# Kernel optimization log

Measured on AMD Instinct MI355X. Metric: run time of the kernel, lower is better.

## Reference

```python
import jax, jax.numpy as jnp
import numpy as np

GS = 256          # group_size
KER = 17          # depthwise conv kernel size (MossFormer ConvModule)

def layer_norm(x, g, b):
    mu = jnp.mean(x, -1, keepdims=True)
    var = jnp.mean(jnp.square(x - mu), -1, keepdims=True)
    return (x - mu) * jax.lax.rsqrt(var + 1e-5) * g + b

def dwconv(x, kernel):
    # x: (B, N, C), kernel: (C, 1, K); depthwise 'same' conv
    p = (KER - 1) // 2
    y = jax.lax.conv_general_dilated(
        jnp.swapaxes(x, 1, 2), kernel, (1,), [(p, p)],
        feature_group_count=x.shape[-1],
        dimension_numbers=('NCH', 'OIH', 'NCH'))
    return jnp.swapaxes(y, 1, 2)

def ffconvm(x, g, b, w, bias, kernel):
    # LayerNorm -> Linear -> SiLU -> ConvModule (residual depthwise conv); dropout = identity (eval)
    h = jax.nn.silu(layer_norm(x, g, b) @ w + bias)
    return h + dwconv(h, kernel)

def flash(x, inv_n, params, n):
    (th_ln_g, th_ln_b, th_w, th_b, th_conv,
     qk_ln_g, qk_ln_b, qk_w, qk_b, qk_conv,
     os_gamma, os_beta,
     out_ln_g, out_ln_b, out_w, out_b, out_conv) = params
    residual = x
    # shift tokens: shift first half of channels forward by one step
    x_shift, x_pass = jnp.split(x, 2, axis=-1)
    x_shift = jnp.pad(x_shift, ((0, 0), (1, 0), (0, 0)))[:, :-1]
    nx = jnp.concatenate([x_shift, x_pass], axis=-1)

    h = ffconvm(nx, th_ln_g, th_ln_b, th_w, th_b, th_conv)      # (1, n, 2048)
    v, u = jnp.split(h, 2, axis=-1)                             # each (1, n, 1024)
    qk = ffconvm(nx, qk_ln_g, qk_ln_b, qk_w, qk_b, qk_conv)     # (1, n, 128)
    qs = qk[..., None, :] * os_gamma + os_beta                  # (1, n, 4, 128)
    quad_q, lin_q, quad_k, lin_k = (qs[..., i, :] for i in range(4))

    # local quadratic attention over groups of GS (n % GS == 0 -> no padding path)
    G = n // GS
    grp = lambda t: t.reshape(1, G, GS, t.shape[-1])
    qq, kk, vg, ug = grp(quad_q), grp(quad_k), grp(v), grp(u)
    sim = jnp.einsum('bgid,bgjd->bgij', qq, kk) * (1.0 / GS)
    attn = jnp.square(jax.nn.relu(sim))                          # relu(sim)**2
    quad_v = jnp.einsum('bgij,bgje->bgie', attn, vg).reshape(1, n, -1)
    quad_u = jnp.einsum('bgij,bgje->bgie', attn, ug).reshape(1, n, -1)

    # global linear attention (non-causal: single global kv summary)
    lin_kv = jnp.einsum('bnd,bne->bde', lin_k, v) * inv_n        # (1, 128, 1024)
    lin_ku = jnp.einsum('bnd,bne->bde', lin_k, u) * inv_n
    lin_v = jnp.einsum('bnd,bde->bne', lin_q, lin_kv)
    lin_u = jnp.einsum('bnd,bde->bne', lin_q, lin_ku)

    att_v = quad_v + lin_v
    att_u = quad_u + lin_u
    out = att_u * v * jax.nn.sigmoid(att_v * u)                  # gated mixing
    return residual + ffconvm(out, out_ln_g, out_ln_b, out_w, out_b, out_conv)

def setup_inputs():
    key = jax.random.key(0)
    ks = jax.random.split(key, 8)
    N, D, H2, QK = 16384, 512, 2048, 128
    s = 0.02
    return dict(
        x=jax.random.normal(ks[0], (1, N, D), jnp.float32),
        inv_n=jnp.float32(1.0 / N),
        th_ln_g=jnp.ones((D,), jnp.float32),
        th_ln_b=jnp.zeros((D,), jnp.float32),
        th_w=jax.random.normal(ks[1], (D, H2), jnp.float32) * s,
        th_b=jnp.zeros((H2,), jnp.float32),
        th_conv=jax.random.normal(ks[2], (H2, 1, KER), jnp.float32) * s,
        qk_ln_g=jnp.ones((D,), jnp.float32),
        qk_ln_b=jnp.zeros((D,), jnp.float32),
        qk_w=jax.random.normal(ks[3], (D, QK), jnp.float32) * s,
        qk_b=jnp.zeros((QK,), jnp.float32),
        qk_conv=jax.random.normal(ks[4], (QK, 1, KER), jnp.float32) * s,
        os_gamma=jax.random.normal(ks[5], (4, QK), jnp.float32) * s,
        os_beta=jnp.zeros((4, QK), jnp.float32),
        out_ln_g=jnp.ones((2 * D,), jnp.float32),
        out_ln_b=jnp.zeros((2 * D,), jnp.float32),
        out_w=jax.random.normal(ks[6], (2 * D, D), jnp.float32) * s,
        out_b=jnp.zeros((D,), jnp.float32),
        out_conv=jax.random.normal(ks[7], (D, 1, KER), jnp.float32) * s,
        n=16384,
    )

def reference(x, inv_n, th_ln_g, th_ln_b, th_w, th_b, th_conv,
              qk_ln_g, qk_ln_b, qk_w, qk_b, qk_conv, os_gamma, os_beta,
              out_ln_g, out_ln_b, out_w, out_b, out_conv, n):
    params = (th_ln_g, th_ln_b, th_w, th_b, th_conv,
              qk_ln_g, qk_ln_b, qk_w, qk_b, qk_conv,
              os_gamma, os_beta,
              out_ln_g, out_ln_b, out_w, out_b, out_conv)
    return flash(x, inv_n, params, n)
```

## Files before the change

### kernel.cpp

```cpp
#include <hip/hip_runtime.h>
#include <math.h>

#define GSZ 256

typedef unsigned short u16;
typedef short bf16x8 __attribute__((ext_vector_type(8)));
typedef u16 u16x8 __attribute__((ext_vector_type(8)));
typedef float f32x4 __attribute__((ext_vector_type(4)));
#define MFMA16 __builtin_amdgcn_mfma_f32_16x16x32_bf16


__device__ __forceinline__ float bf2f(u16 u){
  union { unsigned int i; float f; } x; x.i = ((unsigned int)u) << 16; return x.f;
}
__device__ __forceinline__ u16 f2bf(float f){
  union { float ff; unsigned int i; } x; x.ff = f;
  unsigned int r = x.i + 0x7fffu + ((x.i >> 16) & 1u);
  return (u16)(r >> 16);
}
__device__ __forceinline__ float sigm(float x){ return 1.0f/(1.0f+__expf(-x)); }
__device__ __forceinline__ float siluf(float x){ return x/(1.0f+__expf(-x)); }

__device__ __forceinline__ void gload16(const void* g, void* l){
  __builtin_amdgcn_global_load_lds(
      (const __attribute__((address_space(1))) void*)g,
      (__attribute__((address_space(3))) void*)l, 16, 0, 0);
}

__device__ __forceinline__ float2 blockReduce2(float s, float ss){
  __shared__ float red[8];
  #pragma unroll
  for (int off=32; off>0; off>>=1){
    s  += __shfl_down(s, off, 64);
    ss += __shfl_down(ss, off, 64);
  }
  int lane = threadIdx.x & 63, wid = threadIdx.x >> 6;
  if (lane==0){ red[wid]=s; red[4+wid]=ss; }
  __syncthreads();
  float2 r;
  r.x = red[0]+red[1]+red[2]+red[3];
  r.y = red[4]+red[5]+red[6]+red[7];
  return r;
}


__global__ __launch_bounds__(256) void shift_ln_kernel(
    const float* __restrict__ x, u16* __restrict__ out, int N)
{
  int n = blockIdx.x;
  int t = threadIdx.x;
  float v0 = (n > 0) ? x[(long long)(n-1)*512 + t] : 0.0f;
  float v1 = x[(long long)n*512 + 256 + t];
  float2 r = blockReduce2(v0+v1, fmaf(v0,v0,v1*v1));
  float mu = r.x * (1.0f/512.0f);
  float var = r.y * (1.0f/512.0f) - mu*mu;
  float rs = rsqrtf(var + 1e-5f);
  long long base = (long long)n*512;
  out[base + t]       = f2bf((v0-mu)*rs);
  out[base + 256 + t] = f2bf((v1-mu)*rs);
}

__global__ __launch_bounds__(256) void fuse_wT_kernel(
    const float* __restrict__ g, const float* __restrict__ w,
    u16* __restrict__ wT, int K, int Nn)
{
  __shared__ float sL[32][33];
  int k0 = blockIdx.x*32, n0 = blockIdx.y*32;
  int t = threadIdx.x;
  int r = t >> 3, cq = t & 7;
  float4 v = *(const float4*)(w + (size_t)(k0+r)*Nn + n0 + cq*4);
  float gg = g[k0+r];
  sL[r][cq*4+0] = v.x*gg; sL[r][cq*4+1] = v.y*gg;
  sL[r][cq*4+2] = v.z*gg; sL[r][cq*4+3] = v.w*gg;
  __syncthreads();
  ushort4 o;
  o.x = f2bf(sL[cq*4+0][r]); o.y = f2bf(sL[cq*4+1][r]);
  o.z = f2bf(sL[cq*4+2][r]); o.w = f2bf(sL[cq*4+3][r]);
  *(ushort4*)(wT + (size_t)(n0+r)*K + k0 + cq*4) = o;
}

__global__ void copy_bias_kernel(const float* __restrict__ bias, float* __restrict__ bout, int Nn){
  int i = blockIdx.x*256 + threadIdx.x;
  if (i < Nn) bout[i] = bias[i];
}

__global__ __launch_bounds__(256) void fuse_b_acc(
    const float* __restrict__ bln, const float* __restrict__ w,
    float* __restrict__ bout, int K, int Nn)
{
  int n = blockIdx.x*256 + threadIdx.x;
  int k0 = blockIdx.y*64;
  if (n >= Nn) return;
  float acc = 0.f;
  #pragma unroll
  for (int k = 0; k < 64; ++k)
    acc = fmaf(bln[k0+k], w[(size_t)(k0+k)*Nn + n], acc);
  atomicAdd(&bout[n], acc);
}

__global__ void zero_kernel(float* __restrict__ p, long long total){
  long long i = (long long)blockIdx.x*256 + threadIdx.x;
  if (i < total) p[i] = 0.0f;
}


__global__ __launch_bounds__(256) void gemm_mfma_silu(
    const u16* __restrict__ A, int lda,
    const u16* __restrict__ BT, int ldbt, int wtc0,
    u16* __restrict__ C, int ldc,
    const float* __restrict__ bias, int K)
{
  __shared__ u16 lds[3*16*512];
  int t = threadIdx.x;
  int lane = t & 63, wid = t >> 6;
  int wm = wid >> 1, wn = wid & 1;
  int lrow = lane & 15, kcL = lane >> 4;
  int bm = blockIdx.y*128, bn = blockIdx.x*128;
  const u16* gA0 = A + (size_t)(bm + wid*16 + lrow)*lda + kcL*8;
  const u16* gA1 = A + (size_t)(bm + (wid+4)*16 + lrow)*lda + kcL*8;
  const u16* gB0 = BT + (size_t)(wtc0 + bn + wid*16 + lrow)*ldbt + kcL*8;
  const u16* gB1 = BT + (size_t)(wtc0 + bn + (wid+4)*16 + lrow)*ldbt + kcL*8;
  f32x4 acc[4][4] = {};
  int nt = K >> 5;
  auto issue = [&](int ti, u16* b){
    int k1 = ti << 5;
    gload16(gA0 + k1, b + (size_t)wid*512);
    gload16(gA1 + k1, b + (size_t)(wid+4)*512);
    gload16(gB0 + k1, b + (size_t)(8+wid)*512);
    gload16(gB1 + k1, b + (size_t)(12+wid)*512);
  };
  issue(0, lds);
  if (nt > 1) issue(1, lds + 8192);
  for (int ti = 0; ti < nt; ++ti) {
    if (ti + 2 < nt) {
      issue(ti + 2, lds + (size_t)((ti+2)%3)*8192);
      asm volatile("s_waitcnt vmcnt(8)" ::: "memory");
    } else if (ti + 1 < nt) {
      asm volatile("s_waitcnt vmcnt(4)" ::: "memory");
    } else {
      asm volatile("s_waitcnt vmcnt(0)" ::: "memory");
    }
    __builtin_amdgcn_s_barrier();
    asm volatile("" ::: "memory");
    const bf16x8* L = (const bf16x8*)(lds + (size_t)(ti%3)*8192);
    bf16x8 af[4], bfr[4];
    #pragma unroll
    for (int mr = 0; mr < 4; ++mr) af[mr] = L[(wm*4+mr)*64 + lane];
    #pragma unroll
    for (int nr = 0; nr < 4; ++nr) bfr[nr] = L[(8 + wn*4+nr)*64 + lane];
    #pragma unroll
    for (int mr = 0; mr < 4; ++mr)
      #pragma unroll
      for (int nr = 0; nr < 4; ++nr)
        acc[mr][nr] = MFMA16(af[mr], bfr[nr], acc[mr][nr], 0, 0, 0);
    asm volatile("" ::: "memory");
    __builtin_amdgcn_s_barrier();
  }
  #pragma unroll
  for (int mr = 0; mr < 4; ++mr)
    #pragma unroll
    for (int nr = 0; nr < 4; ++nr) {
      int col = bn + wn*64 + nr*16 + lrow;
      float bs = bias[wtc0 + col];
      #pragma unroll
      for (int i = 0; i < 4; ++i) {
        int row = bm + wm*64 + mr*16 + kcL*4 + i;
        C[(size_t)row*ldc + col] = f2bf(siluf(acc[mr][nr][i] + bs));
      }
    }
}

__global__ __launch_bounds__(256) void score_mfma2(
    const u16* __restrict__ Eq0, const u16* __restrict__ Ek2,
    u16* __restrict__ attn)
{
  __shared__ u16 lds[3*16*512];
  int t = threadIdx.x;
  int lane = t & 63, wid = t >> 6;
  int wm = wid >> 1, wn = wid & 1;
  int lrow = lane & 15, kcL = lane >> 4;
  int g = blockIdx.z;
  int bm = blockIdx.y*128, bn = blockIdx.x*128;
  size_t rowbase = (size_t)g * GSZ;
  const u16* gA0 = Eq0 + (rowbase + bm + wid*16 + lrow)*128 + kcL*8;
  const u16* gA1 = Eq0 + (rowbase + bm + (wid+4)*16 + lrow)*128 + kcL*8;
  const u16* gB0 = Ek2 + (rowbase + bn + wid*16 + lrow)*128 + kcL*8;
  const u16* gB1 = Ek2 + (rowbase + bn + (wid+4)*16 + lrow)*128 + kcL*8;
  f32x4 acc[4][4] = {};
  auto issue = [&](int ti, u16* b){
    int k1 = ti << 5;
    gload16(gA0 + k1, b + (size_t)wid*512);
    gload16(gA1 + k1, b + (size_t)(wid+4)*512);
    gload16(gB0 + k1, b + (size_t)(8+wid)*512);
    gload16(gB1 + k1, b + (size_t)(12+wid)*512);
  };
  issue(0, lds);
  issue(1, lds + 8192);
  for (int ti = 0; ti < 4; ++ti) {
    if (ti + 2 < 4) {
      issue(ti + 2, lds + (size_t)((ti+2)%3)*8192);
      asm volatile("s_waitcnt vmcnt(8)" ::: "memory");
    } else if (ti + 1 < 4) {
      asm volatile("s_waitcnt vmcnt(4)" ::: "memory");
    } else {
      asm volatile("s_waitcnt vmcnt(0)" ::: "memory");
    }
    __builtin_amdgcn_s_barrier();
    asm volatile("" ::: "memory");
    const bf16x8* L = (const bf16x8*)(lds + (size_t)(ti%3)*8192);
    bf16x8 af[4], bfr[4];
    #pragma unroll
    for (int mr = 0; mr < 4; ++mr) af[mr] = L[(wm*4+mr)*64 + lane];
    #pragma unroll
    for (int nr = 0; nr < 4; ++nr) bfr[nr] = L[(8 + wn*4+nr)*64 + lane];
    #pragma unroll
    for (int mr = 0; mr < 4; ++mr)
      #pragma unroll
      for (int nr = 0; nr < 4; ++nr)
        acc[mr][nr] = MFMA16(af[mr], bfr[nr], acc[mr][nr], 0, 0, 0);
    asm volatile("" ::: "memory");
    __builtin_amdgcn_s_barrier();
  }
  #pragma unroll
  for (int mr = 0; mr < 4; ++mr)
    #pragma unroll
    for (int nr = 0; nr < 4; ++nr) {
      int col = bn + wn*64 + nr*16 + lrow;
      #pragma unroll
      for (int i = 0; i < 4; ++i) {
        int row = bm + wm*64 + mr*16 + kcL*4 + i;
        float s = fmaxf(acc[mr][nr][i] * (1.0f/GSZ), 0.0f);
        attn[(rowbase + row)*GSZ + col] = f2bf(s*s);
      }
    }
}

__global__ __launch_bounds__(256) void linkv_mfma(
    const u16* __restrict__ EqkF, const u16* __restrict__ hF,
    float* __restrict__ Fraw, int N)
{
  __shared__ u16 lds[2*12*512];
  int t = threadIdx.x;
  int lane = t & 63, wid = t >> 6;
  int wm = wid >> 1, wn = wid & 1;
  int lrow = lane & 15, kcL = lane >> 4;
  int e0 = blockIdx.x * 64;
  int nkt = (N / gridDim.y) >> 5;
  size_t kt0 = (size_t)blockIdx.y * nkt;
  f32x4 acc[4][2] = {};
  auto issue = [&](int kt, u16* b) {
    size_t ktile = kt0 + kt;
    gload16(EqkF + ((ktile*8 + wid)*64 + lane)*8,           b + (size_t)wid*512);
    gload16(EqkF + ((ktile*8 + wid+4)*64 + lane)*8,         b + (size_t)(wid+4)*512);
    gload16(hF + ((ktile*128 + (e0>>4) + wid)*64 + lane)*8, b + (size_t)(8+wid)*512);
  };
  issue(0, lds);
  int cur = 0;
  for (int ti = 0; ti < nkt; ++ti) {
    if (ti + 1 < nkt) {
      issue(ti + 1, lds + (size_t)(cur^1)*6144);
      asm volatile("s_waitcnt vmcnt(3)" ::: "memory");
    } else {
      asm volatile("s_waitcnt vmcnt(0)" ::: "memory");
    }
    __builtin_amdgcn_s_barrier();
    asm volatile("" ::: "memory");
    const bf16x8* L = (const bf16x8*)(lds + (size_t)cur*6144);
    bf16x8 af[4], bfr[2];
    #pragma unroll
    for (int mr = 0; mr < 4; ++mr) af[mr] = L[(wm*4+mr)*64 + lane];
    #pragma unroll
    for (int nr = 0; nr < 2; ++nr) bfr[nr] = L[(8 + wn*2+nr)*64 + lane];
    #pragma unroll
    for (int mr = 0; mr < 4; ++mr)
      #pragma unroll
      for (int nr = 0; nr < 2; ++nr)
        acc[mr][nr] = MFMA16(af[mr], bfr[nr], acc[mr][nr], 0, 0, 0);
    asm volatile("" ::: "memory");
    __builtin_amdgcn_s_barrier();
    cur ^= 1;
  }
  #pragma unroll
  for (int mr = 0; mr < 4; ++mr)
    #pragma unroll
    for (int nr = 0; nr < 2; ++nr) {
      int e = e0 + wn*32 + nr*16 + lrow;
      #pragma unroll
      for (int i = 0; i < 4; ++i) {
        int d = wm*64 + mr*16 + kcL*4 + i;
        atomicAdd(&Fraw[(size_t)d*2048 + e], acc[mr][nr][i]);
      }
    }
}

__global__ __launch_bounds__(256) void fconv_kernel(
    const float* __restrict__ Fraw, const float* __restrict__ osg, const float* __restrict__ osb,
    const float* __restrict__ hsum, float inv_n,
    u16* __restrict__ FTg, float* __restrict__ cvec)
{
  __shared__ float g1s[128], b1s[128], g3s[128], b3s[128];
  int t = threadIdx.x;
  if (t < 128) { g1s[t] = osg[128+t]; b1s[t] = osb[128+t];
                 g3s[t] = osg[3*128+t]; b3s[t] = osb[3*128+t]; }
  __syncthreads();
  int e = blockIdx.x*256 + t;
  float hs = hsum[e];
  float c = 0.f;
  for (int d = 0; d < 128; ++d) {
    float f = inv_n * fmaf(g3s[d], Fraw[(size_t)d*2048 + e], b3s[d]*hs);
    c = fmaf(b1s[d], f, c);
    FTg[(size_t)e*128 + d] = f2bf(g1s[d] * f);
  }
  cvec[e] = c;
}

__global__ __launch_bounds__(256) void quadlin_mfma(
    const u16* __restrict__ attn, const u16* __restrict__ hF,
    const u16* __restrict__ eqk, const u16* __restrict__ FTg,
    const float* __restrict__ cvec, u16* __restrict__ T2)
{
  __shared__ u16 lds[3*16*512];
  int bid = blockIdx.x;
  int wgid = (bid & 7)*256 + (bid >> 3);
  int g = wgid >> 5;
  int rem = wgid & 31;
  int bm = (rem >> 4) * 128;
  int cb = (rem & 15) * 64;
  int t = threadIdx.x;
  int lane = t & 63, wid = t >> 6;
  int wm = wid >> 1, wn = wid & 1;
  int lrow = lane & 15, kcL = lane >> 4;
  size_t rowbase = (size_t)g * GSZ;
  f32x4 accV[4][2] = {}, accU[4][2] = {};
  const u16* gA0q = attn + (rowbase + bm + wid*16 + lrow)*GSZ + kcL*8;
  const u16* gA1q = attn + (rowbase + bm + (wid+4)*16 + lrow)*GSZ + kcL*8;
  const u16* gA0l = eqk + (rowbase + bm + wid*16 + lrow)*128 + kcL*8;
  const u16* gA1l = eqk + (rowbase + bm + (wid+4)*16 + lrow)*128 + kcL*8;
  const u16* gBVl = FTg + (size_t)(cb + wid*16 + lrow)*128 + kcL*8;
  const u16* gBUl = FTg + (size_t)(1024 + cb + wid*16 + lrow)*128 + kcL*8;
  auto issue = [&](int ti, u16* b) {
    if (ti < 8) {
      int k0 = ti << 5;
      size_t ktile = (size_t)g*8 + ti;
      gload16(gA0q + k0, b + (size_t)wid*512);
      gload16(gA1q + k0, b + (size_t)(wid+4)*512);
      gload16(hF + ((ktile*128 + (cb>>4) + wid)*64 + lane)*8,      b + (size_t)(8+wid)*512);
      gload16(hF + ((ktile*128 + 64 + (cb>>4) + wid)*64 + lane)*8, b + (size_t)(12+wid)*512);
    } else {
      int k0 = (ti - 8) << 5;
      gload16(gA0l + k0, b + (size_t)wid*512);
      gload16(gA1l + k0, b + (size_t)(wid+4)*512);
      gload16(gBVl + k0, b + (size_t)(8+wid)*512);
      gload16(gBUl + k0, b + (size_t)(12+wid)*512);
    }
  };
  issue(0, lds);
  issue(1, lds + 8192);
  for (int ti = 0; ti < 12; ++ti) {
    if (ti + 2 < 12) {
      issue(ti + 2, lds + (size_t)((ti+2)%3)*8192);
      asm volatile("s_waitcnt vmcnt(8)" ::: "memory");
    } else if (ti + 1 < 12) {
      asm volatile("s_waitcnt vmcnt(4)" ::: "memory");
    } else {
      asm volatile("s_waitcnt vmcnt(0)" ::: "memory");
    }
    __builtin_amdgcn_s_barrier();
    asm volatile("" ::: "memory");
    const bf16x8* L = (const bf16x8*)(lds + (size_t)(ti%3)*8192);
    bf16x8 af[4], bv[2], bu[2];
    #pragma unroll
    for (int mr = 0; mr < 4; ++mr) af[mr] = L[(wm*4+mr)*64 + lane];
    #pragma unroll
    for (int nr = 0; nr < 2; ++nr) { bv[nr] = L[(8 + wn*2+nr)*64 + lane];
                                     bu[nr] = L[(12 + wn*2+nr)*64 + lane]; }
    #pragma unroll
    for (int mr = 0; mr < 4; ++mr)
      #pragma unroll
      for (int nr = 0; nr < 2; ++nr) {
        accV[mr][nr] = MFMA16(af[mr], bv[nr], accV[mr][nr], 0, 0, 0);
        accU[mr][nr] = MFMA16(af[mr], bu[nr], accU[mr][nr], 0, 0, 0);
      }
    asm volatile("" ::: "memory");
    __builtin_amdgcn_s_barrier();
  }
  #pragma unroll
  for (int mr = 0; mr < 4; ++mr)
    #pragma unroll
    for (int nr = 0; nr < 2; ++nr) {
      int c = cb + wn*32 + nr*16 + lrow;
      float cV = cvec[c], cU = cvec[1024 + c];
      int np = bm + wm*64 + mr*16 + kcL*4;
      size_t ktile = (size_t)g*8 + (np>>5);
      int lofs = ((np>>3)&3)*16 + (c&15);
      int eo = np & 7;
      ushort4 vq = *(const ushort4*)(hF + ((ktile*128 + (c>>4))*64 + lofs)*8 + eo);
      ushort4 uq = *(const ushort4*)(hF + ((ktile*128 + 64 + (c>>4))*64 + lofs)*8 + eo);
      float vv[4] = {bf2f(vq.x), bf2f(vq.y), bf2f(vq.z), bf2f(vq.w)};
      float uu[4] = {bf2f(uq.x), bf2f(uq.y), bf2f(uq.z), bf2f(uq.w)};
      #pragma unroll
      for (int i = 0; i < 4; ++i) {
        float av = accV[mr][nr][i] + cV;
        float au = accU[mr][nr][i] + cU;
        T2[(rowbase + np + i)*1024 + c] = f2bf(au * vv[i] * sigm(av * uu[i]));
      }
    }
}


__global__ __launch_bounds__(256) void dwconv_hf64(
    const u16* __restrict__ xin, int ldin, const float* __restrict__ kern,
    u16* __restrict__ hF, int colbase, float* __restrict__ hsum, int N)
{
  __shared__ float tile[80][64];
  __shared__ float psum[4][64];
  int c0 = blockIdx.x * 64;
  int n0 = blockIdx.y * 64;
  int t = threadIdx.x;
  int tx = t & 63, ty = t >> 6;
  #pragma unroll
  for (int it = 0; it < 5; ++it) {
    int idx = t + it*256;
    int r = idx >> 4, cq = (idx & 15)*4;
    int gn = n0 - 8 + r;
    float4 f;
    if (gn >= 0 && gn < N) {
      ushort4 q = *(const ushort4*)(xin + (size_t)gn*ldin + c0 + cq);
      f.x = bf2f(q.x); f.y = bf2f(q.y); f.z = bf2f(q.z); f.w = bf2f(q.w);
    } else { f.x = 0.f; f.y = 0.f; f.z = 0.f; f.w = 0.f; }
    *(float4*)&tile[r][cq] = f;
  }
  __syncthreads();
  int chl = c0 + tx;
  float kr[17];
  #pragma unroll
  for (int k = 0; k < 17; ++k) kr[k] = kern[chl*17 + k];
  int c = colbase + chl;
  float loc = 0.f;
  #pragma unroll
  for (int u = 0; u < 2; ++u) {
    u16x8 o;
    #pragma unroll
    for (int rr = 0; rr < 8; ++rr) {
      int r = ty*16 + u*8 + rr;
      float s = 0.0f;
      #pragma unroll
      for (int k = 0; k < 17; ++k) s = fmaf(kr[k], tile[r+k][tx], s);
      float val = tile[r+8][tx] + s;
      loc += val;
      o[rr] = f2bf(val);
    }
    int nn = n0 + ty*16 + u*8;
    *(u16x8*)(hF + ((((size_t)(nn>>5))*128 + (c>>4))*64 + ((nn>>3)&3)*16 + (c&15))*8) = o;
  }
  psum[ty][tx] = loc;
  __syncthreads();
  if (t < 64)
    atomicAdd(&hsum[colbase + c0 + t], psum[0][t]+psum[1][t]+psum[2][t]+psum[3][t]);
}

__global__ __launch_bounds__(256) void dwconv_qk(
    const u16* __restrict__ xin, const float* __restrict__ kern,
    const float* __restrict__ osg, const float* __restrict__ osb,
    u16* __restrict__ Eqk, u16* __restrict__ Eq0, u16* __restrict__ Ek2,
    u16* __restrict__ EqkF, int N)
{
  __shared__ float tile[48][64];
  int c0 = blockIdx.x * 64;
  int n0 = blockIdx.y * 32;
  int t = threadIdx.x;
  int tx = t & 63, ty = t >> 6;
  #pragma unroll
  for (int it = 0; it < 3; ++it) {
    int idx = t + it*256;
    int r = idx >> 4, cq = (idx & 15)*4;
    int gn = n0 - 8 + r;
    float4 f;
    if (gn >= 0 && gn < N) {
      ushort4 q = *(const ushort4*)(xin + (size_t)gn*128 + c0 + cq);
      f.x = bf2f(q.x); f.y = bf2f(q.y); f.z = bf2f(q.z); f.w = bf2f(q.w);
    } else { f.x = 0.f; f.y = 0.f; f.z = 0.f; f.w = 0.f; }
    *(float4*)&tile[r][cq] = f;
  }
  __syncthreads();
  int ch = c0 + tx;
  float kr[17];
  #pragma unroll
  for (int k = 0; k < 17; ++k) kr[k] = kern[ch*17 + k];
  float g0 = osg[ch], b0 = osb[ch];
  float g2 = osg[2*128+ch], b2 = osb[2*128+ch];
  float vals[8];
  #pragma unroll
  for (int rr = 0; rr < 8; ++rr) {
    int r = ty*8 + rr;
    float s = 0.0f;
    #pragma unroll
    for (int k = 0; k < 17; ++k) s = fmaf(kr[k], tile[r+k][tx], s);
    vals[rr] = tile[r+8][tx] + s;
    size_t gi = (size_t)(n0 + r)*128 + ch;
    Eqk[gi] = f2bf(vals[rr]);
    Eq0[gi] = f2bf(fmaf(vals[rr], g0, b0));
    Ek2[gi] = f2bf(fmaf(vals[rr], g2, b2));
  }
  u16x8 o;
  #pragma unroll
  for (int rr = 0; rr < 8; ++rr) o[rr] = f2bf(vals[rr]);
  *(u16x8*)(EqkF + ((((size_t)(n0>>5))*8 + (ch>>4))*64 + ty*16 + (ch&15))*8) = o;
}

__global__ __launch_bounds__(256) void dwconv_final64(
    const u16* __restrict__ xin, const float* __restrict__ kern,
    const float* __restrict__ resid, float* __restrict__ y, int N)
{
  __shared__ float tile[80][64];
  int c0 = blockIdx.x * 64;
  int n0 = blockIdx.y * 64;
  int t = threadIdx.x;
  int tx = t & 63, ty = t >> 6;
  #pragma unroll
  for (int it = 0; it < 5; ++it) {
    int idx = t + it*256;
    int r = idx >> 4, cq = (idx & 15)*4;
    int gn = n0 - 8 + r;
    float4 f;
    if (gn >= 0 && gn < N) {
      ushort4 q = *(const ushort4*)(xin + (size_t)gn*512 + c0 + cq);
      f.x = bf2f(q.x); f.y = bf2f(q.y); f.z = bf2f(q.z); f.w = bf2f(q.w);
    } else { f.x = 0.f; f.y = 0.f; f.z = 0.f; f.w = 0.f; }
    *(float4*)&tile[r][cq] = f;
  }
  __syncthreads();
  int ch = c0 + tx;
  float kr[17];
  #pragma unroll
  for (int k = 0; k < 17; ++k) kr[k] = kern[ch*17 + k];
  #pragma unroll
  for (int rr = 0; rr < 16; ++rr) {
    int r = ty*16 + rr;
    float s = 0.0f;
    #pragma unroll
    for (int k = 0; k < 17; ++k) s = fmaf(kr[k], tile[r+k][tx], s);
    size_t gi = (size_t)(n0 + r)*512 + ch;
    y[gi] = resid[gi] + tile[r+8][tx] + s;
  }
}

__global__ __launch_bounds__(256) void ln1024_kernel(u16* __restrict__ buf)
{
  long long n = blockIdx.x;
  ushort4* p = (ushort4*)(buf + n*1024) + threadIdx.x;
  ushort4 q = *p;
  float a = bf2f(q.x), b = bf2f(q.y), c = bf2f(q.z), d = bf2f(q.w);
  float s = a+b+c+d;
  float ss = fmaf(a,a, fmaf(b,b, fmaf(c,c, d*d)));
  float2 r = blockReduce2(s, ss);
  float mu = r.x * (1.0f/1024.0f);
  float var = r.y * (1.0f/1024.0f) - mu*mu;
  float rs = rsqrtf(var + 1e-5f);
  q.x = f2bf((a-mu)*rs); q.y = f2bf((b-mu)*rs);
  q.z = f2bf((c-mu)*rs); q.w = f2bf((d-mu)*rs);
  *p = q;
}


extern "C" void kernel_launch(void* const* d_in, const int* in_sizes, int n_in,
                              void* d_out, int out_size, void* d_ws, size_t ws_size,
                              hipStream_t stream)
{
  const float* x        = (const float*)d_in[0];
  const float* th_ln_g  = (const float*)d_in[2];
  const float* th_ln_b  = (const float*)d_in[3];
  const float* th_w     = (const float*)d_in[4];
  const float* th_b     = (const float*)d_in[5];
  const float* th_conv  = (const float*)d_in[6];
  const float* qk_ln_g  = (const float*)d_in[7];
  const float* qk_ln_b  = (const float*)d_in[8];
  const float* qk_w     = (const float*)d_in[9];
  const float* qk_b     = (const float*)d_in[10];
  const float* qk_conv  = (const float*)d_in[11];
  const float* osg      = (const float*)d_in[12];
  const float* osb      = (const float*)d_in[13];
  const float* out_ln_g = (const float*)d_in[14];
  const float* out_ln_b = (const float*)d_in[15];
  const float* out_w    = (const float*)d_in[16];
  const float* out_b    = (const float*)d_in[17];
  const float* out_conv = (const float*)d_in[18];

  const int N = in_sizes[0] / 512;
  const float inv_n = 1.0f / (float)N;
  const int G = N / GSZ;
  char* wsb = (char*)d_ws;

  size_t o_hF   = 0;
  size_t o_T2   = o_hF  + (size_t)N*2048*2;
  size_t o_C    = o_T2  + (size_t)N*1024*2;
  size_t o_eqk  = o_C   + (size_t)N*512*2;
  size_t o_fr   = o_eqk + (size_t)N*128*2;
  size_t o_wth  = o_fr  + (size_t)N*128*2;
  size_t o_wqk  = o_wth + (size_t)2048*512*2;
  size_t o_wout = o_wqk + (size_t)128*512*2;
  size_t o_bth  = o_wout+ (size_t)1024*512*2;
  size_t o_bqk  = o_bth + 2048*4;
  size_t o_bout = o_bqk + 128*4;
  size_t o_hsum = o_bout + 512*4;
  size_t required = o_hsum + 2048*4;
  if (ws_size < required) return;

  u16*   hF   = (u16*)(wsb + o_hF);
  u16*   T2   = (u16*)(wsb + o_T2);
  u16*   Hpre = T2;
  u16*   Cu   = (u16*)(wsb + o_C);
  u16*   nx   = Cu;
  u16*   EqkF = Cu;
  u16*   Eq0  = Cu + (size_t)N*256;
  u16*   Ek2  = Cu + (size_t)N*384;
  u16*   attn = Cu;
  u16*   outtmp = Cu;
  u16*   Eqk  = (u16*)(wsb + o_eqk);
  u16*   Dqk  = (u16*)(wsb + o_fr);
  float* Fraw = (float*)(wsb + o_fr);
  u16*   FTg  = (u16*)(wsb + o_fr + (size_t)128*2048*4);
  float* cvec = (float*)(wsb + o_fr + (size_t)128*2048*4 + (size_t)2048*128*2);
  u16*   WthT = (u16*)(wsb + o_wth);
  u16*   WqkT = (u16*)(wsb + o_wqk);
  u16*   WoutT= (u16*)(wsb + o_wout);
  float* Bth  = (float*)(wsb + o_bth);
  float* Bqk  = (float*)(wsb + o_bqk);
  float* Bout = (float*)(wsb + o_bout);
  float* hsum = (float*)(wsb + o_hsum);

  hipLaunchKernelGGL(fuse_wT_kernel, dim3(16, 64), dim3(256), 0, stream, th_ln_g, th_w, WthT, 512, 2048);
  hipLaunchKernelGGL(fuse_wT_kernel, dim3(16, 4),  dim3(256), 0, stream, qk_ln_g, qk_w, WqkT, 512, 128);
  hipLaunchKernelGGL(fuse_wT_kernel, dim3(32, 16), dim3(256), 0, stream, out_ln_g, out_w, WoutT, 1024, 512);
  hipLaunchKernelGGL(copy_bias_kernel, dim3(8), dim3(256), 0, stream, th_b, Bth, 2048);
  hipLaunchKernelGGL(copy_bias_kernel, dim3(1), dim3(256), 0, stream, qk_b, Bqk, 128);
  hipLaunchKernelGGL(copy_bias_kernel, dim3(2), dim3(256), 0, stream, out_b, Bout, 512);
  hipLaunchKernelGGL(fuse_b_acc, dim3(8, 8),  dim3(256), 0, stream, th_ln_b,  th_w,  Bth, 512, 2048);
  hipLaunchKernelGGL(fuse_b_acc, dim3(1, 8),  dim3(256), 0, stream, qk_ln_b,  qk_w,  Bqk, 512, 128);
  hipLaunchKernelGGL(fuse_b_acc, dim3(2, 16), dim3(256), 0, stream, out_ln_b, out_w, Bout, 1024, 512);
  hipLaunchKernelGGL(zero_kernel, dim3(8), dim3(256), 0, stream, hsum, 2048LL);

  hipLaunchKernelGGL(shift_ln_kernel, dim3(N), dim3(256), 0, stream, x, nx, N);

  for (int sc = 0; sc < 2; ++sc) {
    hipLaunchKernelGGL(gemm_mfma_silu, dim3(8, N/128), dim3(256), 0, stream,
                       nx, 512, WthT, 512, sc*1024, Hpre, 1024, Bth, 512);
    hipLaunchKernelGGL(dwconv_hf64, dim3(16, N/64), dim3(256), 0, stream,
                       Hpre, 1024, th_conv + (size_t)sc*1024*17, hF, sc*1024, hsum, N);
  }

  hipLaunchKernelGGL(gemm_mfma_silu, dim3(1, N/128), dim3(256), 0, stream,
                     nx, 512, WqkT, 512, 0, Dqk, 128, Bqk, 512);
  hipLaunchKernelGGL(dwconv_qk, dim3(2, N/32), dim3(256), 0, stream,
                     Dqk, qk_conv, osg, osb, Eqk, Eq0, Ek2, EqkF, N);

  hipLaunchKernelGGL(zero_kernel, dim3(1024), dim3(256), 0, stream, Fraw, (long long)128*2048);
  hipLaunchKernelGGL(linkv_mfma, dim3(32, 16), dim3(256), 0, stream, EqkF, hF, Fraw, N);
  hipLaunchKernelGGL(fconv_kernel, dim3(8), dim3(256), 0, stream, Fraw, osg, osb, hsum, inv_n, FTg, cvec);

  hipLaunchKernelGGL(score_mfma2, dim3(2, 2, G), dim3(256), 0, stream, Eq0, Ek2, attn);

  hipLaunchKernelGGL(quadlin_mfma, dim3(2*G*16), dim3(256), 0, stream,
                     attn, hF, Eqk, FTg, cvec, T2);

  hipLaunchKernelGGL(ln1024_kernel, dim3(N), dim3(256), 0, stream, T2);
  hipLaunchKernelGGL(gemm_mfma_silu, dim3(4, N/128), dim3(256), 0, stream,
                     T2, 1024, WoutT, 1024, 0, outtmp, 512, Bout, 1024);
  hipLaunchKernelGGL(dwconv_final64, dim3(8, N/64), dim3(256), 0, stream,
                     outtmp, out_conv, x, (float*)d_out, N);
}
```

Baseline: 383.2 us.

## Fold output LayerNorm into GEMM epilogue via row stats; double-buffer quadlin LDS

The in-place normalisation pass over T2 is replaced by a kernel that only computes each row's mean and rstd. The output GEMM now applies the normalisation algebraically in its epilogue as r*(acc - mu*S) + bias, where S is the column sum of the gamma-scaled weights. This removes the write-back of the 1024-wide normalised rows. The quadlin kernel also drops from triple to double LDS buffering, which may help occupancy but gives less prefetch depth. Feeding unnormalised bf16 activations into the GEMM changes rounding and risks cancellation in the subtraction.

New measurement: 392.6 us. 1.02x slower.

```diff
diff --git a/kernel.cpp b/kernel.cpp
--- a/kernel.cpp
+++ b/kernel.cpp
@@ -101,6 +101,24 @@
 __global__ void zero_kernel(float* __restrict__ p, long long total){
   long long i = (long long)blockIdx.x*256 + threadIdx.x;
   if (i < total) p[i] = 0.0f;
+}
+
+__global__ __launch_bounds__(256) void rowstat_kernel(
+    const u16* __restrict__ buf, float* __restrict__ mu, float* __restrict__ rs)
+{
+  long long n = blockIdx.x;
+  const ushort4* p = (const ushort4*)(buf + n*1024) + threadIdx.x;
+  ushort4 q = *p;
+  float a = bf2f(q.x), b = bf2f(q.y), c = bf2f(q.z), d = bf2f(q.w);
+  float s = a+b+c+d;
+  float ss = fmaf(a,a, fmaf(b,b, fmaf(c,c, d*d)));
+  float2 r = blockReduce2(s, ss);
+  if (threadIdx.x == 0) {
+    float m = r.x * (1.0f/1024.0f);
+    float var = r.y * (1.0f/1024.0f) - m*m;
+    mu[n] = m;
+    rs[n] = rsqrtf(var + 1e-5f);
+  }
 }
 
 
@@ -166,6 +184,75 @@
       for (int i = 0; i < 4; ++i) {
         int row = bm + wm*64 + mr*16 + kcL*4 + i;
         C[(size_t)row*ldc + col] = f2bf(siluf(acc[mr][nr][i] + bs));
+      }
+    }
+}
+
+__global__ __launch_bounds__(256) void gemm_mfma_ln_silu(
+    const u16* __restrict__ A, int lda,
+    const u16* __restrict__ BT, int ldbt,
+    u16* __restrict__ C, int ldc,
+    const float* __restrict__ bias, const float* __restrict__ S,
+    const float* __restrict__ mu, const float* __restrict__ rs, int K)
+{
+  __shared__ u16 lds[3*16*512];
+  int t = threadIdx.x;
+  int lane = t & 63, wid = t >> 6;
+  int wm = wid >> 1, wn = wid & 1;
+  int lrow = lane & 15, kcL = lane >> 4;
+  int bm = blockIdx.y*128, bn = blockIdx.x*128;
+  const u16* gA0 = A + (size_t)(bm + wid*16 + lrow)*lda + kcL*8;
+  const u16* gA1 = A + (size_t)(bm + (wid+4)*16 + lrow)*lda + kcL*8;
+  const u16* gB0 = BT + (size_t)(bn + wid*16 + lrow)*ldbt + kcL*8;
+  const u16* gB1 = BT + (size_t)(bn + (wid+4)*16 + lrow)*ldbt + kcL*8;
+  f32x4 acc[4][4] = {};
+  int nt = K >> 5;
+  auto issue = [&](int ti, u16* b){
+    int k1 = ti << 5;
+    gload16(gA0 + k1, b + (size_t)wid*512);
+    gload16(gA1 + k1, b + (size_t)(wid+4)*512);
+    gload16(gB0 + k1, b + (size_t)(8+wid)*512);
+    gload16(gB1 + k1, b + (size_t)(12+wid)*512);
+  };
+  issue(0, lds);
+  issue(1, lds + 8192);
+  for (int ti = 0; ti < nt; ++ti) {
+    if (ti + 2 < nt) {
+      issue(ti + 2, lds + (size_t)((ti+2)%3)*8192);
+      asm volatile("s_waitcnt vmcnt(8)" ::: "memory");
+    } else if (ti + 1 < nt) {
+      asm volatile("s_waitcnt vmcnt(4)" ::: "memory");
+    } else {
+      asm volatile("s_waitcnt vmcnt(0)" ::: "memory");
+    }
+    __builtin_amdgcn_s_barrier();
+    asm volatile("" ::: "memory");
+    const bf16x8* L = (const bf16x8*)(lds + (size_t)(ti%3)*8192);
+    bf16x8 af[4], bfr[4];
+    #pragma unroll
+    for (int mr = 0; mr < 4; ++mr) af[mr] = L[(wm*4+mr)*64 + lane];
+    #pragma unroll
+    for (int nr = 0; nr < 4; ++nr) bfr[nr] = L[(8 + wn*4+nr)*64 + lane];
+    #pragma unroll
+    for (int mr = 0; mr < 4; ++mr)
+      #pragma unroll
+      for (int nr = 0; nr < 4; ++nr)
+        acc[mr][nr] = MFMA16(af[mr], bfr[nr], acc[mr][nr], 0, 0, 0);
+    asm volatile("" ::: "memory");
+    __builtin_amdgcn_s_barrier();
+  }
+  #pragma unroll
+  for (int mr = 0; mr < 4; ++mr)
+    #pragma unroll
+    for (int nr = 0; nr < 4; ++nr) {
+      int col = bn + wn*64 + nr*16 + lrow;
+      float bs = bias[col];
+      float Sc = S[col];
+      #pragma unroll
+      for (int i = 0; i < 4; ++i) {
+        int row = bm + wm*64 + mr*16 + kcL*4 + i;
+        float m = mu[row], r = rs[row];
+        C[(size_t)row*ldc + col] = f2bf(siluf(fmaf(r, acc[mr][nr][i] - m*Sc, bs)));
       }
     }
 }
@@ -319,7 +406,7 @@
     const u16* __restrict__ eqk, const u16* __restrict__ FTg,
     const float* __restrict__ cvec, u16* __restrict__ T2)
 {
-  __shared__ u16 lds[3*16*512];
+  __shared__ u16 lds[2*16*512];
   int bid = blockIdx.x;
   int wgid = (bid & 7)*256 + (bid >> 3);
   int g = wgid >> 5;
@@ -355,19 +442,17 @@
     }
   };
   issue(0, lds);
-  issue(1, lds + 8192);
+  int cur = 0;
   for (int ti = 0; ti < 12; ++ti) {
-    if (ti + 2 < 12) {
-      issue(ti + 2, lds + (size_t)((ti+2)%3)*8192);
-      asm volatile("s_waitcnt vmcnt(8)" ::: "memory");
-    } else if (ti + 1 < 12) {
+    if (ti + 1 < 12) {
+      issue(ti + 1, lds + (size_t)(cur^1)*8192);
       asm volatile("s_waitcnt vmcnt(4)" ::: "memory");
     } else {
       asm volatile("s_waitcnt vmcnt(0)" ::: "memory");
     }
     __builtin_amdgcn_s_barrier();
     asm volatile("" ::: "memory");
-    const bf16x8* L = (const bf16x8*)(lds + (size_t)(ti%3)*8192);
+    const bf16x8* L = (const bf16x8*)(lds + (size_t)cur*8192);
     bf16x8 af[4], bv[2], bu[2];
     #pragma unroll
     for (int mr = 0; mr < 4; ++mr) af[mr] = L[(wm*4+mr)*64 + lane];
@@ -383,6 +468,7 @@
       }
     asm volatile("" ::: "memory");
     __builtin_amdgcn_s_barrier();
+    cur ^= 1;
   }
   #pragma unroll
   for (int mr = 0; mr < 4; ++mr)
@@ -543,23 +629,6 @@
     size_t gi = (size_t)(n0 + r)*512 + ch;
     y[gi] = resid[gi] + tile[r+8][tx] + s;
   }
-}
-
-__global__ __launch_bounds__(256) void ln1024_kernel(u16* __restrict__ buf)
-{
-  long long n = blockIdx.x;
-  ushort4* p = (ushort4*)(buf + n*1024) + threadIdx.x;
-  ushort4 q = *p;
-  float a = bf2f(q.x), b = bf2f(q.y), c = bf2f(q.z), d = bf2f(q.w);
-  float s = a+b+c+d;
-  float ss = fmaf(a,a, fmaf(b,b, fmaf(c,c, d*d)));
-  float2 r = blockReduce2(s, ss);
-  float mu = r.x * (1.0f/1024.0f);
-  float var = r.y * (1.0f/1024.0f) - mu*mu;
-  float rs = rsqrtf(var + 1e-5f);
-  q.x = f2bf((a-mu)*rs); q.y = f2bf((b-mu)*rs);
-  q.z = f2bf((c-mu)*rs); q.w = f2bf((d-mu)*rs);
-  *p = q;
 }
 
 
@@ -603,7 +672,10 @@
   size_t o_bqk  = o_bth + 2048*4;
   size_t o_bout = o_bqk + 128*4;
   size_t o_hsum = o_bout + 512*4;
-  size_t required = o_hsum + 2048*4;
+  size_t o_S    = o_hsum + 2048*4;
+  size_t o_mu   = o_S    + 512*4;
+  size_t o_rs   = o_mu   + (size_t)N*4;
+  size_t required = o_rs + (size_t)N*4;
   if (ws_size < required) return;
 
   u16*   hF   = (u16*)(wsb + o_hF);
@@ -628,6 +700,9 @@
   float* Bqk  = (float*)(wsb + o_bqk);
   float* Bout = (float*)(wsb + o_bout);
   float* hsum = (float*)(wsb + o_hsum);
+  float* Svec = (float*)(wsb + o_S);
+  float* muv  = (float*)(wsb + o_mu);
+  float* rsv  = (float*)(wsb + o_rs);
 
   hipLaunchKernelGGL(fuse_wT_kernel, dim3(16, 64), dim3(256), 0, stream, th_ln_g, th_w, WthT, 512, 2048);
   hipLaunchKernelGGL(fuse_wT_kernel, dim3(16, 4),  dim3(256), 0, stream, qk_ln_g, qk_w, WqkT, 512, 128);
@@ -639,6 +714,8 @@
   hipLaunchKernelGGL(fuse_b_acc, dim3(1, 8),  dim3(256), 0, stream, qk_ln_b,  qk_w,  Bqk, 512, 128);
   hipLaunchKernelGGL(fuse_b_acc, dim3(2, 16), dim3(256), 0, stream, out_ln_b, out_w, Bout, 1024, 512);
   hipLaunchKernelGGL(zero_kernel, dim3(8), dim3(256), 0, stream, hsum, 2048LL);
+  hipLaunchKernelGGL(zero_kernel, dim3(2), dim3(256), 0, stream, Svec, 512LL);
+  hipLaunchKernelGGL(fuse_b_acc, dim3(2, 16), dim3(256), 0, stream, out_ln_g, out_w, Svec, 1024, 512);
 
   hipLaunchKernelGGL(shift_ln_kernel, dim3(N), dim3(256), 0, stream, x, nx, N);
 
@@ -663,9 +740,9 @@
   hipLaunchKernelGGL(quadlin_mfma, dim3(2*G*16), dim3(256), 0, stream,
                      attn, hF, Eqk, FTg, cvec, T2);
 
-  hipLaunchKernelGGL(ln1024_kernel, dim3(N), dim3(256), 0, stream, T2);
-  hipLaunchKernelGGL(gemm_mfma_silu, dim3(4, N/128), dim3(256), 0, stream,
-                     T2, 1024, WoutT, 1024, 0, outtmp, 512, Bout, 1024);
+  hipLaunchKernelGGL(rowstat_kernel, dim3(N), dim3(256), 0, stream, T2, muv, rsv);
+  hipLaunchKernelGGL(gemm_mfma_ln_silu, dim3(4, N/128), dim3(256), 0, stream,
+                     T2, 1024, WoutT, 1024, outtmp, 512, Bout, Svec, muv, rsv, 1024);
   hipLaunchKernelGGL(dwconv_final64, dim3(8, N/64), dim3(256), 0, stream,
                      outtmp, out_conv, x, (float*)d_out, N);
 }
```
